# Kernel optimization log

Measured on AMD Instinct MI355X. Metric: run time of the kernel, lower is better.

Reference implementation:

```python
import jax, jax.numpy as jnp
import numpy as np

ALPHA = 0.2  # LeakyReLU negative slope
NEG = -9e15

def setup_inputs() -> dict:
    key = jax.random.key(0)
    k1, k2, k3, k4 = jax.random.split(key, 4)
    N, F_in, F_out = 8192, 512, 64
    x = jax.random.normal(k1, (N, F_in), dtype=jnp.float32)
    adj_mat = jax.random.randint(k2, (N, N), 0, 2, dtype=jnp.int32)
    w = jax.random.normal(k3, (F_in, F_out), dtype=jnp.float32) * (2.0 / (F_in + F_out)) ** 0.5
    a = jax.random.normal(k4, (2 * F_out, 1), dtype=jnp.float32) * (2.0 / (2 * F_out + 1)) ** 0.5
    return {"x": x, "adj_mat": adj_mat, "w": w, "a": a}

def reference(x, adj_mat, w, a):
    F_out = w.shape[1]
    wh = x @ w                      # [N, F_out]
    # Decompose concat([wh_i, wh_j]) @ a into two rank-1 score vectors (same math)
    a1, a2 = a[:F_out, 0], a[F_out:, 0]
    e = (wh @ a1)[:, None] + (wh @ a2)[None, :]        # [N, N]
    e = jnp.where(e > 0, e, ALPHA * e)                 # leakyrelu
    attn = jnp.where(adj_mat > 0, e, NEG)
    attn = jax.nn.softmax(attn, axis=1)                # dropout p=0 -> identity
    h_prime = attn @ wh                                # [N, F_out]
    return jnp.where(h_prime > 0, h_prime, jnp.expm1(h_prime))  # elu
```

## Files before the change

kernel.cpp:

```cpp
#include <hip/hip_runtime.h>
#include <hip/hip_bf16.h>

#define ALPHA 0.2f
#define NN 8192
#define FIN 512
#define FOUT 64

typedef __attribute__((ext_vector_type(8))) __bf16 bf16x8;
typedef __attribute__((ext_vector_type(4))) float f32x4;

__global__ __launch_bounds__(256) void k_wh(
    const float* __restrict__ x, const float* __restrict__ w,
    const float* __restrict__ a, float* __restrict__ wh,
    float* __restrict__ s1, float* __restrict__ s2) {
  __shared__ float xs[128][64];
  __shared__ float part1[64][4];
  __shared__ float part2[64][4];
  const int t = threadIdx.x;
  const int r = t & 63;
  const int cg = __builtin_amdgcn_readfirstlane(t >> 6);
  const int row0 = blockIdx.x * 64;

  float acc[16];
#pragma unroll
  for (int u = 0; u < 16; u++) acc[u] = 0.f;

  const int srow = t >> 2;
  const int scol = (t & 3) * 32;

  for (int kc = 0; kc < 4; kc++) {
#pragma unroll
    for (int it = 0; it < 8; it++) {
      float4 v = *(const float4*)(x + (size_t)(row0 + srow) * FIN + kc * 128 + scol + it * 4);
      xs[scol + it * 4 + 0][srow] = v.x;
      xs[scol + it * 4 + 1][srow] = v.y;
      xs[scol + it * 4 + 2][srow] = v.z;
      xs[scol + it * 4 + 3][srow] = v.w;
    }
    __syncthreads();
    const float* wp = w + (size_t)kc * 128 * FOUT + cg * 16;
    for (int kk = 0; kk < 128; kk++) {
      float av = xs[kk][r];
#pragma unroll
      for (int u = 0; u < 16; u++) acc[u] = fmaf(av, wp[kk * 64 + u], acc[u]);
    }
    __syncthreads();
  }

#pragma unroll
  for (int u4 = 0; u4 < 4; u4++) {
    float4 v;
    v.x = acc[u4 * 4 + 0]; v.y = acc[u4 * 4 + 1];
    v.z = acc[u4 * 4 + 2]; v.w = acc[u4 * 4 + 3];
    *(float4*)(wh + (size_t)(row0 + r) * FOUT + cg * 16 + u4 * 4) = v;
  }

  float p1 = 0.f, p2 = 0.f;
#pragma unroll
  for (int u = 0; u < 16; u++) {
    p1 = fmaf(acc[u], a[cg * 16 + u], p1);
    p2 = fmaf(acc[u], a[FOUT + cg * 16 + u], p2);
  }
  part1[r][cg] = p1;
  part2[r][cg] = p2;
  __syncthreads();
  if (t < 64) {
    s1[row0 + t] = part1[t][0] + part1[t][1] + part1[t][2] + part1[t][3];
    s2[row0 + t] = part2[t][0] + part2[t][1] + part2[t][2] + part2[t][3];
  }
}

__global__ __launch_bounds__(256) void k_pack(
    const float* __restrict__ wh, uint4* __restrict__ packB) {
  const int tg = blockIdx.x * 256 + threadIdx.x;
  const int lane = tg & 63;
  const int cg = (tg >> 6) & 3;
  const int q = tg >> 8;
  const int jrow = q * 32 + ((lane >> 4) * 8);
  const int col = cg * 16 + (lane & 15);
  bf16x8 v;
#pragma unroll
  for (int s = 0; s < 8; s++)
    v[s] = (__bf16)wh[(size_t)(jrow + s) * FOUT + col];
  packB[tg] = __builtin_bit_cast(uint4, v);
}

__global__ __launch_bounds__(256) void k_attn(
    const int* __restrict__ adj, const float* __restrict__ s1,
    const float* __restrict__ s2, const uint4* __restrict__ packB,
    float* __restrict__ out) {
  __shared__ float s2s[NN];
  __shared__ float accp[4][16][64];
  __shared__ float lp[4][16];
  __shared__ float wred[4];

  const int t = threadIdx.x;
  const int wv = t >> 6;
  const int lane = t & 63;

  float m = -1e30f;
#pragma unroll
  for (int it = 0; it < 8; it++) {
    int i4 = t + it * 256;
    float4 v = *(const float4*)&s2[i4 * 4];
    *(float4*)&s2s[i4 * 4] = v;
    m = fmaxf(m, fmaxf(fmaxf(v.x, v.y), fmaxf(v.z, v.w)));
  }
#pragma unroll
  for (int off = 32; off; off >>= 1) m = fmaxf(m, __shfl_xor(m, off));
  if (lane == 0) wred[wv] = m;
  __syncthreads();
  const float s2max = fmaxf(fmaxf(wred[0], wred[1]), fmaxf(wred[2], wred[3]));

  const int m16 = lane & 15;
  const int kb = lane >> 4;
  const int row0 = blockIdx.x * 16;
  const int i = row0 + m16;
  const float s1v = s1[i];
  float sh = s1v + s2max;
  sh = fmaxf(sh, ALPHA * sh);

  f32x4 acc0 = {0.f, 0.f, 0.f, 0.f};
  f32x4 acc1 = {0.f, 0.f, 0.f, 0.f};
  f32x4 acc2 = {0.f, 0.f, 0.f, 0.f};
  f32x4 acc3 = {0.f, 0.f, 0.f, 0.f};
  float lsum = 0.f;

  const int4* adjp = (const int4*)(adj + (size_t)i * NN) + (wv * 512 + kb * 2);
  const uint4* bp = packB + (size_t)(wv * 64) * 256 + lane;
  int jj = wv * 2048 + kb * 8;

  for (int q = 0; q < 64; q++) {
    const int4 A0 = adjp[0];
    const int4 A1 = adjp[1];
    adjp += 8;
    const float4 S0 = *(const float4*)&s2s[jj];
    const float4 S1 = *(const float4*)&s2s[jj + 4];
    jj += 32;
    const uint4 B0 = bp[0];
    const uint4 B1 = bp[64];
    const uint4 B2 = bp[128];
    const uint4 B3 = bp[192];
    bp += 256;

    float sv[8] = {S0.x, S0.y, S0.z, S0.w, S1.x, S1.y, S1.z, S1.w};
    int av[8] = {A0.x, A0.y, A0.z, A0.w, A1.x, A1.y, A1.z, A1.w};
    bf16x8 af;
#pragma unroll
    for (int v = 0; v < 8; v++) {
      float e = s1v + sv[v];
      float lr = fmaxf(e, ALPHA * e);
      float pv = __expf(lr - sh);
      pv = (av[v] > 0) ? pv : 0.f;
      lsum += pv;
      af[v] = (__bf16)pv;
    }
    acc0 = __builtin_amdgcn_mfma_f32_16x16x32_bf16(af, __builtin_bit_cast(bf16x8, B0), acc0, 0, 0, 0);
    acc1 = __builtin_amdgcn_mfma_f32_16x16x32_bf16(af, __builtin_bit_cast(bf16x8, B1), acc1, 0, 0, 0);
    acc2 = __builtin_amdgcn_mfma_f32_16x16x32_bf16(af, __builtin_bit_cast(bf16x8, B2), acc2, 0, 0, 0);
    acc3 = __builtin_amdgcn_mfma_f32_16x16x32_bf16(af, __builtin_bit_cast(bf16x8, B3), acc3, 0, 0, 0);
  }

  lsum += __shfl_xor(lsum, 16);
  lsum += __shfl_xor(lsum, 32);
  if (lane < 16) lp[wv][lane] = lsum;

#pragma unroll
  for (int rg = 0; rg < 4; rg++) {
    accp[wv][kb * 4 + rg][0 * 16 + m16] = acc0[rg];
    accp[wv][kb * 4 + rg][1 * 16 + m16] = acc1[rg];
    accp[wv][kb * 4 + rg][2 * 16 + m16] = acc2[rg];
    accp[wv][kb * 4 + rg][3 * 16 + m16] = acc3[rg];
  }
  __syncthreads();

#pragma unroll
  for (int u = 0; u < 4; u++) {
    int idx = t + u * 256;
    int rr = idx >> 6;
    int cc = idx & 63;
    float s = accp[0][rr][cc] + accp[1][rr][cc] + accp[2][rr][cc] + accp[3][rr][cc];
    float l = lp[0][rr] + lp[1][rr] + lp[2][rr] + lp[3][rr];
    float h = s / l;
    out[(size_t)(row0 + rr) * FOUT + cc] = (h > 0.f) ? h : (__expf(h) - 1.f);
  }
}

extern "C" void kernel_launch(void* const* d_in, const int* in_sizes, int n_in,
                              void* d_out, int out_size, void* d_ws, size_t ws_size,
                              hipStream_t stream) {
  const float* x = (const float*)d_in[0];
  const int* adj = (const int*)d_in[1];
  const float* w = (const float*)d_in[2];
  const float* a = (const float*)d_in[3];
  float* out = (float*)d_out;

  char* ws = (char*)d_ws;
  float* wh = (float*)ws;
  float* s1 = (float*)(ws + (size_t)NN * FOUT * 4);
  float* s2 = s1 + NN;
  uint4* packB = (uint4*)(ws + (size_t)NN * FOUT * 4 + 2 * (size_t)NN * 4);

  k_wh<<<dim3(128), dim3(256), 0, stream>>>(x, w, a, wh, s1, s2);
  k_pack<<<dim3(256), dim3(256), 0, stream>>>(wh, packB);
  k_attn<<<dim3(512), dim3(256), 0, stream>>>(adj, s1, s2, packB, out);
}
```

Before: 453.9 us.

## Fuse bf16 packing into projection kernel and split attention over eight waves

The separate pack kernel and the fp32 wh buffer are removed. The projection kernel now converts its accumulators to bf16 in shared memory and writes the MFMA-ready packed layout directly, which saves a launch and a global round trip. The attention kernel moves to 512 threads, with each of 8 waves covering 1024 columns instead of 4 waves covering 2048, to add parallelism and latency hiding per block. In exchange it needs more shared memory for the partial accumulators and a longer 8-way reduction. The inner projection loop also gets an unroll-4 pragma.

Result: no change. 460.9 us (+1.5%).

```diff
diff --git a/kernel.cpp b/kernel.cpp
--- a/kernel.cpp
+++ b/kernel.cpp
@@ -11,9 +11,10 @@
 
 __global__ __launch_bounds__(256) void k_wh(
     const float* __restrict__ x, const float* __restrict__ w,
-    const float* __restrict__ a, float* __restrict__ wh,
-    float* __restrict__ s1, float* __restrict__ s2) {
+    const float* __restrict__ a, float* __restrict__ s1,
+    float* __restrict__ s2, uint4* __restrict__ packB) {
   __shared__ float xs[128][64];
+  __shared__ unsigned short tile[64][68];
   __shared__ float part1[64][4];
   __shared__ float part2[64][4];
   const int t = threadIdx.x;
@@ -39,20 +40,13 @@
     }
     __syncthreads();
     const float* wp = w + (size_t)kc * 128 * FOUT + cg * 16;
+#pragma unroll 4
     for (int kk = 0; kk < 128; kk++) {
       float av = xs[kk][r];
 #pragma unroll
       for (int u = 0; u < 16; u++) acc[u] = fmaf(av, wp[kk * 64 + u], acc[u]);
     }
     __syncthreads();
-  }
-
-#pragma unroll
-  for (int u4 = 0; u4 < 4; u4++) {
-    float4 v;
-    v.x = acc[u4 * 4 + 0]; v.y = acc[u4 * 4 + 1];
-    v.z = acc[u4 * 4 + 2]; v.w = acc[u4 * 4 + 3];
-    *(float4*)(wh + (size_t)(row0 + r) * FOUT + cg * 16 + u4 * 4) = v;
   }
 
   float p1 = 0.f, p2 = 0.f;
@@ -63,36 +57,41 @@
   }
   part1[r][cg] = p1;
   part2[r][cg] = p2;
+
+#pragma unroll
+  for (int u = 0; u < 16; u++) {
+    __bf16 b = (__bf16)acc[u];
+    tile[r][cg * 16 + u] = __builtin_bit_cast(unsigned short, b);
+  }
   __syncthreads();
+
   if (t < 64) {
     s1[row0 + t] = part1[t][0] + part1[t][1] + part1[t][2] + part1[t][3];
     s2[row0 + t] = part2[t][0] + part2[t][1] + part2[t][2] + part2[t][3];
   }
+
+  const int lane = t & 63;
+  const int cgw = t >> 6;
+  const int col = cgw * 16 + (lane & 15);
+#pragma unroll
+  for (int e = 0; e < 2; e++) {
+    const int rloc = e * 32 + ((lane >> 4) * 8);
+    bf16x8 v;
+#pragma unroll
+    for (int s = 0; s < 8; s++)
+      v[s] = __builtin_bit_cast(__bf16, tile[rloc + s][col]);
+    packB[(size_t)(((row0 >> 5) + e) * 4 + cgw) * 64 + lane] = __builtin_bit_cast(uint4, v);
+  }
 }
 
-__global__ __launch_bounds__(256) void k_pack(
-    const float* __restrict__ wh, uint4* __restrict__ packB) {
-  const int tg = blockIdx.x * 256 + threadIdx.x;
-  const int lane = tg & 63;
-  const int cg = (tg >> 6) & 3;
-  const int q = tg >> 8;
-  const int jrow = q * 32 + ((lane >> 4) * 8);
-  const int col = cg * 16 + (lane & 15);
-  bf16x8 v;
-#pragma unroll
-  for (int s = 0; s < 8; s++)
-    v[s] = (__bf16)wh[(size_t)(jrow + s) * FOUT + col];
-  packB[tg] = __builtin_bit_cast(uint4, v);
-}
-
-__global__ __launch_bounds__(256) void k_attn(
+__global__ __launch_bounds__(512) void k_attn(
     const int* __restrict__ adj, const float* __restrict__ s1,
     const float* __restrict__ s2, const uint4* __restrict__ packB,
     float* __restrict__ out) {
   __shared__ float s2s[NN];
-  __shared__ float accp[4][16][64];
-  __shared__ float lp[4][16];
-  __shared__ float wred[4];
+  __shared__ float accp[8][16][64];
+  __shared__ float lp[8][16];
+  __shared__ float wred[8];
 
   const int t = threadIdx.x;
   const int wv = t >> 6;
@@ -100,8 +99,8 @@
 
   float m = -1e30f;
 #pragma unroll
-  for (int it = 0; it < 8; it++) {
-    int i4 = t + it * 256;
+  for (int it = 0; it < 4; it++) {
+    int i4 = t + it * 512;
     float4 v = *(const float4*)&s2[i4 * 4];
     *(float4*)&s2s[i4 * 4] = v;
     m = fmaxf(m, fmaxf(fmaxf(v.x, v.y), fmaxf(v.z, v.w)));
@@ -110,7 +109,9 @@
   for (int off = 32; off; off >>= 1) m = fmaxf(m, __shfl_xor(m, off));
   if (lane == 0) wred[wv] = m;
   __syncthreads();
-  const float s2max = fmaxf(fmaxf(wred[0], wred[1]), fmaxf(wred[2], wred[3]));
+  float s2max = wred[0];
+#pragma unroll
+  for (int u = 1; u < 8; u++) s2max = fmaxf(s2max, wred[u]);
 
   const int m16 = lane & 15;
   const int kb = lane >> 4;
@@ -126,11 +127,11 @@
   f32x4 acc3 = {0.f, 0.f, 0.f, 0.f};
   float lsum = 0.f;
 
-  const int4* adjp = (const int4*)(adj + (size_t)i * NN) + (wv * 512 + kb * 2);
-  const uint4* bp = packB + (size_t)(wv * 64) * 256 + lane;
-  int jj = wv * 2048 + kb * 8;
-
-  for (int q = 0; q < 64; q++) {
+  const int4* adjp = (const int4*)(adj + (size_t)i * NN) + (wv * 256 + kb * 2);
+  const uint4* bp = packB + (size_t)(wv * 32) * 256 + lane;
+  int jj = wv * 1024 + kb * 8;
+
+  for (int q = 0; q < 32; q++) {
     const int4 A0 = adjp[0];
     const int4 A1 = adjp[1];
     adjp += 8;
@@ -175,12 +176,16 @@
   __syncthreads();
 
 #pragma unroll
-  for (int u = 0; u < 4; u++) {
-    int idx = t + u * 256;
+  for (int u = 0; u < 2; u++) {
+    int idx = t + u * 512;
     int rr = idx >> 6;
     int cc = idx & 63;
-    float s = accp[0][rr][cc] + accp[1][rr][cc] + accp[2][rr][cc] + accp[3][rr][cc];
-    float l = lp[0][rr] + lp[1][rr] + lp[2][rr] + lp[3][rr];
+    float s = 0.f, l = 0.f;
+#pragma unroll
+    for (int wq = 0; wq < 8; wq++) {
+      s += accp[wq][rr][cc];
+      l += lp[wq][rr];
+    }
     float h = s / l;
     out[(size_t)(row0 + rr) * FOUT + cc] = (h > 0.f) ? h : (__expf(h) - 1.f);
   }
@@ -196,12 +201,10 @@
   float* out = (float*)d_out;
 
   char* ws = (char*)d_ws;
-  float* wh = (float*)ws;
-  float* s1 = (float*)(ws + (size_t)NN * FOUT * 4);
+  float* s1 = (float*)ws;
   float* s2 = s1 + NN;
-  uint4* packB = (uint4*)(ws + (size_t)NN * FOUT * 4 + 2 * (size_t)NN * 4);
-
-  k_wh<<<dim3(128), dim3(256), 0, stream>>>(x, w, a, wh, s1, s2);
-  k_pack<<<dim3(256), dim3(256), 0, stream>>>(wh, packB);
-  k_attn<<<dim3(512), dim3(256), 0, stream>>>(adj, s1, s2, packB, out);
+  uint4* packB = (uint4*)(ws + 2 * (size_t)NN * 4);
+
+  k_wh<<<dim3(128), dim3(256), 0, stream>>>(x, w, a, s1, s2, packB);
+  k_attn<<<dim3(512), dim3(512), 0, stream>>>(adj, s1, s2, packB, out);
 }
```
